# Kernel optimization log

Measured on AMD Instinct MI355X. Metric: run time of the kernel, lower is better.

Reference implementation:

```python
import jax, jax.numpy as jnp
import numpy as np

EPS_GN = 1e-5
EPS_ATTN = 1e-6
HEADS = 4
DIM_HEAD = 32
GROUPS = 32  # min(32, channels=128)


def group_norm(x, weight, bias, groups=GROUPS, eps=EPS_GN):
    # x: [b, c, h, w]
    b, c, h, w = x.shape
    xg = x.reshape(b, groups, c // groups, h, w)
    mean = xg.mean(axis=(2, 3, 4), keepdims=True)
    var = xg.var(axis=(2, 3, 4), keepdims=True)
    xg = (xg - mean) * jax.lax.rsqrt(var + eps)
    x = xg.reshape(b, c, h, w)
    return x * weight[None, :, None, None] + bias[None, :, None, None]


def conv1x1(x, w):
    # x: [b, c, h, w], w: [out, in] -> [b, out, h, w]
    return jnp.einsum('bchw,oc->bohw', x, w)


def setup_inputs() -> dict:
    key = jax.random.key(0)
    ks = jax.random.split(key, 6)
    b, c, h, w = 16, 128, 128, 128
    inner = HEADS * DIM_HEAD  # 128
    x = jax.random.normal(ks[0], (b, c, h, w), dtype=jnp.float32)
    gn1_w = jnp.ones((c,), jnp.float32) + 0.02 * jax.random.normal(ks[1], (c,), jnp.float32)
    gn1_b = 0.02 * jax.random.normal(ks[2], (c,), jnp.float32)
    w_qkv = jax.random.normal(ks[3], (inner * 3, c), jnp.float32) / np.sqrt(c)
    w_out = jax.random.normal(ks[4], (c, inner), jnp.float32) / np.sqrt(inner)
    gn2_w = jnp.ones((c,), jnp.float32) + 0.02 * jax.random.normal(ks[5], (c,), jnp.float32)
    gn2_b = jnp.zeros((c,), jnp.float32)
    return {"x": x, "gn1_w": gn1_w, "gn1_b": gn1_b, "w_qkv": w_qkv,
            "w_out": w_out, "gn2_w": gn2_w, "gn2_b": gn2_b}


def reference(x, gn1_w, gn1_b, w_qkv, w_out, gn2_w, gn2_b):
    b, c, h, w = x.shape
    residual = x
    xn = group_norm(x, gn1_w, gn1_b)
    qkv = conv1x1(xn, w_qkv)                      # [b, 3*inner, h, w]
    q, k, v = jnp.split(qkv, 3, axis=1)
    # 'b (heads d) h w -> b heads (h w) d'
    def to_tokens(t):
        return t.reshape(b, HEADS, DIM_HEAD, h * w).transpose(0, 1, 3, 2)
    q, k, v = to_tokens(q), to_tokens(k), to_tokens(v)
    q = jax.nn.elu(q) + 1.0
    k = jax.nn.elu(k) + 1.0
    k_sum = k.sum(axis=2)                          # [b, heads, d]
    kv = jnp.einsum('bhnd,bhne->bhde', k, v)       # [b, heads, d, d]
    qk_sum = jnp.einsum('bhnd,bhd->bhn', q, k_sum) # [b, heads, n]
    qkv_out = jnp.einsum('bhnd,bhde->bhne', q, kv) # [b, heads, n, d]
    out = qkv_out / (qk_sum[..., None] + EPS_ATTN)
    # 'b heads (h w) d -> b (heads d) h w'
    out = out.transpose(0, 1, 3, 2).reshape(b, HEADS * DIM_HEAD, h, w)
    out = conv1x1(out, w_out)
    out = group_norm(out, gn2_w, gn2_b)
    return out + residual
```

## Files before the change

### kernel.cpp

```cpp
#include <hip/hip_runtime.h>

#define B_   16
#define C_   128
#define HW_  16384

typedef __attribute__((ext_vector_type(4))) float  floatx4;
typedef __attribute__((ext_vector_type(8))) short  short8;
typedef __attribute__((ext_vector_type(4))) short  short4v;

static __device__ __forceinline__ unsigned short f2bf(float f){
  unsigned int u = __float_as_uint(f);
  u += 0x7FFFu + ((u >> 16) & 1u);
  return (unsigned short)(u >> 16);
}
static __device__ __forceinline__ float bf2f(unsigned short h){
  return __uint_as_float(((unsigned int)h) << 16);
}
static __device__ __forceinline__ float elu1(float v){
  return v > 0.f ? v + 1.f : __expf(v);
}
static __device__ __forceinline__ int keyx(int n){ return ((n >> 1) & 7) ^ ((n >> 4) & 7); }

__global__ __launch_bounds__(512) void k_xprep(const float* __restrict__ x,
    unsigned short* __restrict__ xT, float* __restrict__ gn1part){
  int blk = blockIdx.x;
  int b = blk >> 6, tile = blk & 63;
  int n0 = tile * 256;
  __shared__ unsigned short XS[32768];
  int t = threadIdx.x, w = t >> 6, l = t & 63;
  float sk[4], sk2[4];
  #pragma unroll
  for (int k = 0; k < 4; ++k){ sk[k] = 0.f; sk2[k] = 0.f; }
  #pragma unroll
  for (int k = 0; k < 4; ++k){
    float4 f4[4];
    #pragma unroll
    for (int j = 0; j < 4; ++j){
      int c = 16*w + 4*k + j;
      f4[j] = *(const float4*)(x + ((size_t)(b*128 + c))*HW_ + n0 + 4*l);
    }
    #pragma unroll
    for (int j = 0; j < 4; ++j){
      sk[k]  += f4[j].x + f4[j].y + f4[j].z + f4[j].w;
      sk2[k] += f4[j].x*f4[j].x + f4[j].y*f4[j].y + f4[j].z*f4[j].z + f4[j].w*f4[j].w;
    }
    int c0 = 16*w + 4*k, cs = c0 >> 3, co = c0 & 7;
    #pragma unroll
    for (int i = 0; i < 4; ++i){
      int n = 4*l + i;
      short4v p;
      #pragma unroll
      for (int j = 0; j < 4; ++j) p[j] = (short)f2bf(((const float*)&f4[j])[i]);
      *(short4v*)(XS + n*128 + (((cs ^ keyx(n)) << 3) + co)) = p;
    }
  }
  #pragma unroll
  for (int k = 0; k < 4; ++k){
    float a = sk[k], q = sk2[k];
    #pragma unroll
    for (int o = 32; o; o >>= 1){ a += __shfl_down(a, o); q += __shfl_down(q, o); }
    if (l == 0){
      gn1part[((size_t)blk)*64 + (4*w + k)*2 + 0] = a;
      gn1part[((size_t)blk)*64 + (4*w + k)*2 + 1] = q;
    }
  }
  __syncthreads();
  unsigned short* dst = xT + ((size_t)blk)*32768;
  for (int it = 0; it < 8; ++it){
    int slot = t + it*512;
    *(short8*)(dst + slot*8) = *(const short8*)(XS + slot*8);
  }
}

__global__ __launch_bounds__(64) void k_gn1fin(const float* __restrict__ gn1part,
    float* __restrict__ mean, float* __restrict__ rstd){
  int bg = blockIdx.x;
  int b = bg >> 5, g = bg & 31, l = threadIdx.x;
  const float* p = gn1part + ((size_t)(b*64 + l))*64 + g*2;
  float s = p[0], s2 = p[1];
  #pragma unroll
  for (int o = 32; o; o >>= 1){ s += __shfl_down(s, o); s2 += __shfl_down(s2, o); }
  if (l == 0){
    float m = s * (1.f/65536.f);
    float var = s2 * (1.f/65536.f) - m*m;
    mean[bg] = m; rstd[bg] = rsqrtf(var + 1e-5f);
  }
}

__global__ __launch_bounds__(64) void k_fold(const float* __restrict__ wqkv, const float* __restrict__ wout,
    const float* __restrict__ g1w, const float* __restrict__ g1b,
    const float* __restrict__ mean, const float* __restrict__ rstd,
    unsigned short* __restrict__ wqp, float* __restrict__ bias, unsigned short* __restrict__ woutb){
  int i = blockIdx.x, l = threadIdx.x;
  if (i < 6144){
    int b = i / 384, o = i % 384;
    float bsum = 0.f;
    #pragma unroll
    for (int j = 0; j < 2; ++j){
      int c = l*2 + j, g = c >> 2;
      float m = mean[b*32 + g], r = rstd[b*32 + g];
      float A  = r * g1w[c];
      float Bc = g1b[c] - m * A;
      float wv = wqkv[o*128 + c];
      wqp[((size_t)(b*384 + o))*128 + c] = f2bf(wv * A);
      bsum += wv * Bc;
    }
    #pragma unroll
    for (int o2 = 32; o2; o2 >>= 1) bsum += __shfl_down(bsum, o2);
    if (l == 0) bias[b*384 + o] = bsum;
  } else {
    int r = i - 6144;
    #pragma unroll
    for (int j = 0; j < 2; ++j){ int c = l*2 + j; woutb[r*128 + c] = f2bf(wout[r*128 + c]); }
  }
}

__global__ __launch_bounds__(512) void k_kv(const unsigned short* __restrict__ xT,
    const unsigned short* __restrict__ wqp, const float* __restrict__ bias,
    float* __restrict__ kvpart, float* __restrict__ ksumpart){
  int blk = blockIdx.x;
  int b = blk >> 7, nt = blk & 127;
  __shared__ unsigned short S[32768];
  int t = threadIdx.x, w = t >> 6, lane = t & 63, lr = lane & 15, lk = lane >> 4;
  const unsigned short* src = xT + ((size_t)(b*64 + (nt >> 1)))*32768 + (nt & 1)*16384;
  for (int it = 0; it < 4; ++it){
    int slot = t + it*512;
    *(short8*)(S + slot*8) = *(const short8*)(src + slot*8);
  }
  __syncthreads();
  short8 afr[2][4]; float biasr[2][4];
  #pragma unroll
  for (int rt = 0; rt < 2; ++rt){
    int o = 128 + rt*128 + w*16;
    #pragma unroll
    for (int ks = 0; ks < 4; ++ks)
      afr[rt][ks] = *(const short8*)(wqp + ((size_t)(b*384 + o + lr))*128 + ks*32 + lk*8);
    #pragma unroll
    for (int r = 0; r < 4; ++r) biasr[rt][r] = bias[b*384 + o + lk*4 + r];
  }
  short4v kpk[8], vpk[8];
  for (int ct = 0; ct < 8; ++ct){
    int nr = ct*16 + lr;
    int kn = keyx(nr);
    short8 bfr[4];
    #pragma unroll
    for (int ks = 0; ks < 4; ++ks)
      bfr[ks] = *(const short8*)(S + nr*128 + (((ks*4 + lk) ^ kn) << 3));
    #pragma unroll
    for (int rt = 0; rt < 2; ++rt){
      floatx4 acc = {0.f,0.f,0.f,0.f};
      #pragma unroll
      for (int ks = 0; ks < 4; ++ks)
        acc = __builtin_amdgcn_mfma_f32_16x16x32_bf16(afr[rt][ks], bfr[ks], acc, 0,0,0);
      short4v pk;
      #pragma unroll
      for (int r = 0; r < 4; ++r){
        float v = acc[r] + biasr[rt][r];
        if (rt == 0) v = elu1(v);
        pk[r] = (short)f2bf(v);
      }
      if (rt == 0) kpk[ct] = pk; else vpk[ct] = pk;
    }
  }
  __syncthreads();
  for (int ct = 0; ct < 8; ++ct){
    int n = ct*16 + lr;
    #pragma unroll
    for (int r = 0; r < 4; ++r){
      int c = w*16 + lk*4 + r;
      int key = (c >> 1) & 7;
      int off = c*128 + ((((n >> 3) ^ key) << 3) + (n & 7));
      S[off]         = (unsigned short)kpk[ct][r];
      S[16384 + off] = (unsigned short)vpk[ct][r];
    }
  }
  __syncthreads();
  short8 ones;
  #pragma unroll
  for (int j = 0; j < 8; ++j) ones[j] = (short)0x3F80;
  #pragma unroll
  for (int j = 0; j < 2; ++j){
    int m = w + 8*j;
    int h = m >> 2, dt = (m >> 1) & 1, et = m & 1;
    int arow = h*32 + dt*16 + lr, brow = h*32 + et*16 + lr;
    int akey = (lr >> 1) & 7;
    floatx4 acc = {0.f,0.f,0.f,0.f}, ks_acc = {0.f,0.f,0.f,0.f};
    #pragma unroll
    for (int ks = 0; ks < 4; ++ks){
      short8 ka = *(const short8*)(S + arow*128 + (((ks*4 + lk) ^ akey) << 3));
      short8 vb = *(const short8*)(S + 16384 + brow*128 + (((ks*4 + lk) ^ akey) << 3));
      acc = __builtin_amdgcn_mfma_f32_16x16x32_bf16(ka, vb, acc, 0,0,0);
      if (et == 0) ks_acc = __builtin_amdgcn_mfma_f32_16x16x32_bf16(ka, ones, ks_acc, 0,0,0);
    }
    float* kvp = kvpart + ((size_t)((b*128 + nt)*4 + h))*1024;
    #pragma unroll
    for (int r = 0; r < 4; ++r)
      kvp[(dt*16 + lk*4 + r)*32 + et*16 + lr] = acc[r];
    if (et == 0 && lr == 0){
      float* ksp = ksumpart + ((size_t)((b*128 + nt)*4 + h))*32;
      #pragma unroll
      for (int r = 0; r < 4; ++r) ksp[dt*16 + lk*4 + r] = ks_acc[r];
    }
  }
}

__global__ __launch_bounds__(256) void k_kvfin(const float* __restrict__ kvpart, const float* __restrict__ ksumpart,
    unsigned short* __restrict__ kvF){
  int bh = blockIdx.x, t = threadIdx.x;
  int b = bh >> 2, h = bh & 3;
  __shared__ float kvL[1024];
  __shared__ float ksumL[32];
  for (int i = t; i < 1024; i += 256){
    float s = 0.f;
    for (int nt = 0; nt < 128; ++nt) s += kvpart[((size_t)((b*128 + nt)*4 + h))*1024 + i];
    kvL[i] = s;
  }
  if (t < 32){
    float s = 0.f;
    for (int nt = 0; nt < 128; ++nt) s += ksumpart[((size_t)((b*128 + nt)*4 + h))*32 + t];
    ksumL[t] = s;
  }
  __syncthreads();
  for (int idx = t; idx < 3*512; idx += 256){
    int f = idx >> 9, rem = idx & 511;
    int lane = rem >> 3, j = rem & 7;
    int d = (lane >> 4)*8 + j;
    float v = (f < 2) ? kvL[d*32 + f*16 + (lane & 15)] : ksumL[d];
    kvF[(size_t)(bh*3 + f)*512 + rem] = f2bf(v);
  }
}

__global__ __launch_bounds__(512) void k_attn2(const unsigned short* __restrict__ xT,
    const unsigned short* __restrict__ wqp, const float* __restrict__ bias,
    const unsigned short* __restrict__ kvF, const unsigned short* __restrict__ woutb,
    unsigned short* __restrict__ hb, float* __restrict__ gn2part){
  int blk = blockIdx.x;
  int b = blk >> 6;
  int n0 = (blk & 63) * 256;
  __shared__ unsigned short S[32768];
  int t = threadIdx.x, w = t >> 6, lane = t & 63, lr = lane & 15, lk = lane >> 4;
  const unsigned short* src = xT + ((size_t)blk)*32768;
  for (int it = 0; it < 8; ++it){
    int slot = t + it*512;
    *(short8*)(S + slot*8) = *(const short8*)(src + slot*8);
  }
  short8 afr[4]; float biasq[4];
  #pragma unroll
  for (int ks = 0; ks < 4; ++ks)
    afr[ks] = *(const short8*)(wqp + ((size_t)(b*384 + w*16 + lr))*128 + ks*32 + lk*8);
  #pragma unroll
  for (int r = 0; r < 4; ++r) biasq[r] = bias[b*384 + w*16 + lk*4 + r];
  __syncthreads();
  short4v qpk[16];
  for (int ct = 0; ct < 16; ++ct){
    int nr = ct*16 + lr;
    int kn = keyx(nr);
    short8 bfr[4];
    #pragma unroll
    for (int ks = 0; ks < 4; ++ks)
      bfr[ks] = *(const short8*)(S + nr*128 + (((ks*4 + lk) ^ kn) << 3));
    floatx4 acc = {0.f,0.f,0.f,0.f};
    #pragma unroll
    for (int ks = 0; ks < 4; ++ks)
      acc = __builtin_amdgcn_mfma_f32_16x16x32_bf16(afr[ks], bfr[ks], acc, 0,0,0);
    short4v pk;
    #pragma unroll
    for (int r = 0; r < 4; ++r) pk[r] = (short)f2bf(elu1(acc[r] + biasq[r]));
    qpk[ct] = pk;
  }
  __syncthreads();
  for (int ct = 0; ct < 16; ++ct){
    int n = ct*16 + lr;
    int c0 = w*16 + lk*4;
    *(short4v*)(S + n*128 + ((((c0 >> 3) ^ (n & 7)) << 3) + (c0 & 7))) = qpk[ct];
  }
  const unsigned short* kvFb = kvF + (size_t)b * 12 * 512;
  short8 kvf[4][2], ksf[4];
  #pragma unroll
  for (int h = 0; h < 4; ++h){
    kvf[h][0] = *(const short8*)(kvFb + (h*3 + 0)*512 + lane*8);
    kvf[h][1] = *(const short8*)(kvFb + (h*3 + 1)*512 + lane*8);
    ksf[h]    = *(const short8*)(kvFb + (h*3 + 2)*512 + lane*8);
  }
  __syncthreads();
  short8 qf[2][4];
  #pragma unroll
  for (int nt = 0; nt < 2; ++nt){
    int n = w*32 + nt*16 + lr;
    #pragma unroll
    for (int h = 0; h < 4; ++h)
      qf[nt][h] = *(const short8*)(S + n*128 + (((4*h + lk) ^ (n & 7)) << 4) / 2);
  }
  #pragma unroll
  for (int nt = 0; nt < 2; ++nt){
    int n_local = w*32 + nt*16 + lr;
    #pragma unroll
    for (int h = 0; h < 4; ++h){
      floatx4 z = {0.f,0.f,0.f,0.f};
      floatx4 dn = __builtin_amdgcn_mfma_f32_16x16x32_bf16(ksf[h],    qf[nt][h], z, 0,0,0);
      floatx4 p0 = __builtin_amdgcn_mfma_f32_16x16x32_bf16(kvf[h][0], qf[nt][h], z, 0,0,0);
      floatx4 p1 = __builtin_amdgcn_mfma_f32_16x16x32_bf16(kvf[h][1], qf[nt][h], z, 0,0,0);
      float inv = 1.f / (dn[0] + 1e-6f);
      short4v o0, o1;
      #pragma unroll
      for (int r = 0; r < 4; ++r){ o0[r] = (short)f2bf(p0[r]*inv); o1[r] = (short)f2bf(p1[r]*inv); }
      int c0 = h*32 + lk*4;
      *(short4v*)(S + n_local*128 + ((((c0 >> 3) ^ (n_local & 7)) << 3) + (c0 & 7))) = o0;
      int c1 = c0 + 16;
      *(short4v*)(S + n_local*128 + ((((c1 >> 3) ^ (n_local & 7)) << 3) + (c1 & 7))) = o1;
    }
  }
  __syncthreads();
  short8 afr2[4];
  #pragma unroll
  for (int ks = 0; ks < 4; ++ks)
    afr2[ks] = *(const short8*)(woutb + (size_t)(w*16 + lr)*128 + ks*32 + lk*8);
  float gs[4] = {0,0,0,0}, gq[4] = {0,0,0,0};
  for (int ct = 0; ct < 16; ++ct){
    int nr = ct*16 + lr;
    short8 bfr[4];
    #pragma unroll
    for (int ks = 0; ks < 4; ++ks)
      bfr[ks] = *(const short8*)(S + nr*128 + (((ks*4 + lk) ^ (nr & 7)) << 3));
    floatx4 acc = {0.f,0.f,0.f,0.f};
    #pragma unroll
    for (int ks = 0; ks < 4; ++ks)
      acc = __builtin_amdgcn_mfma_f32_16x16x32_bf16(afr2[ks], bfr[ks], acc, 0,0,0);
    int nn = n0 + ct*16 + lr;
    #pragma unroll
    for (int r = 0; r < 4; ++r){
      float hv = acc[r];
      hb[((size_t)b*128 + w*16 + lk*4 + r) * HW_ + nn] = f2bf(hv);
      gs[r] += hv; gq[r] += hv * hv;
    }
  }
  #pragma unroll
  for (int m = 1; m < 16; m <<= 1){
    #pragma unroll
    for (int r = 0; r < 4; ++r){ gs[r] += __shfl_xor(gs[r], m); gq[r] += __shfl_xor(gq[r], m); }
  }
  if (lr == 0){
    #pragma unroll
    for (int r = 0; r < 4; ++r){
      int o = w*16 + lk*4 + r;
      gn2part[((size_t)blk*128 + o)*2 + 0] = gs[r];
      gn2part[((size_t)blk*128 + o)*2 + 1] = gq[r];
    }
  }
}

__global__ __launch_bounds__(64) void k_gn2stats(const float* __restrict__ gn2part,
    float* __restrict__ mean, float* __restrict__ rstd){
  int b = blockIdx.x >> 5, g = blockIdx.x & 31;
  int lane = threadIdx.x;
  float s = 0.f, s2 = 0.f;
  #pragma unroll
  for (int j = 0; j < 4; ++j){
    const float* p = gn2part + (((size_t)(b*64 + lane))*128 + g*4 + j)*2;
    s += p[0]; s2 += p[1];
  }
  #pragma unroll
  for (int o = 32; o; o >>= 1){ s += __shfl_down(s, o); s2 += __shfl_down(s2, o); }
  if (lane == 0){
    float m = s * (1.f/65536.f);
    float var = s2 * (1.f/65536.f) - m*m;
    mean[blockIdx.x] = m; rstd[blockIdx.x] = rsqrtf(var + 1e-5f);
  }
}

__global__ __launch_bounds__(256) void k_final(const unsigned short* __restrict__ hb, const float* __restrict__ x,
    float* __restrict__ out,
    const float* __restrict__ mean, const float* __restrict__ rstd,
    const float* __restrict__ g2w, const float* __restrict__ g2b){
  for (size_t chunk = (size_t)blockIdx.x*256 + threadIdx.x; chunk < 4194304ull; chunk += (size_t)2048*256){
    size_t base = chunk * 8;
    int c  = (int)((base >> 14) & 127);
    int bg = (int)(base >> 21) * 32 + (c >> 2);
    float m = mean[bg], r = rstd[bg];
    float sc = r * g2w[c], sh = g2b[c] - m * sc;
    short8 hv = *(const short8*)(hb + base);
    const float4* xp = (const float4*)(x + base);
    float4 x0 = xp[0], x1 = xp[1];
    float4 o0, o1;
    o0.x = bf2f((unsigned short)hv[0])*sc + sh + x0.x;
    o0.y = bf2f((unsigned short)hv[1])*sc + sh + x0.y;
    o0.z = bf2f((unsigned short)hv[2])*sc + sh + x0.z;
    o0.w = bf2f((unsigned short)hv[3])*sc + sh + x0.w;
    o1.x = bf2f((unsigned short)hv[4])*sc + sh + x1.x;
    o1.y = bf2f((unsigned short)hv[5])*sc + sh + x1.y;
    o1.z = bf2f((unsigned short)hv[6])*sc + sh + x1.z;
    o1.w = bf2f((unsigned short)hv[7])*sc + sh + x1.w;
    float4* op = (float4*)(out + base);
    op[0] = o0; op[1] = o1;
  }
}

extern "C" void kernel_launch(void* const* d_in, const int* in_sizes, int n_in,
                              void* d_out, int out_size, void* d_ws, size_t ws_size,
                              hipStream_t stream){
  const float* x    = (const float*)d_in[0];
  const float* g1w  = (const float*)d_in[1];
  const float* g1b  = (const float*)d_in[2];
  const float* wqkv = (const float*)d_in[3];
  const float* wout = (const float*)d_in[4];
  const float* g2w  = (const float*)d_in[5];
  const float* g2b  = (const float*)d_in[6];
  char* ws = (char*)d_ws;
  (void)in_sizes; (void)n_in; (void)out_size; (void)ws_size;

  float* gn1part  = (float*)(ws + 0);
  float* gn1_mean = (float*)(ws + 262144);
  float* gn1_rstd = (float*)(ws + 264192);
  float* gn2_mean = (float*)(ws + 266240);
  float* gn2_rstd = (float*)(ws + 268288);
  float* bias     = (float*)(ws + 270336);
  unsigned short* woutb = (unsigned short*)(ws + 294912);
  unsigned short* kvF   = (unsigned short*)(ws + 327680);
  unsigned short* wqp   = (unsigned short*)(ws + 524288);
  float* ksumpart = (float*)(ws + 2097152);
  float* kvpart   = (float*)(ws + 3145728);
  float* gn2part  = (float*)(ws + 36700160);
  unsigned short* xT = (unsigned short*)(ws + 37748736);
  unsigned short* hb = (unsigned short*)(ws + 104857600);

  k_xprep<<<dim3(1024), dim3(512), 0, stream>>>(x, xT, gn1part);
  k_gn1fin<<<dim3(512), dim3(64), 0, stream>>>(gn1part, gn1_mean, gn1_rstd);
  k_fold<<<dim3(6272), dim3(64), 0, stream>>>(wqkv, wout, g1w, g1b, gn1_mean, gn1_rstd, wqp, bias, woutb);
  k_kv<<<dim3(2048), dim3(512), 0, stream>>>(xT, wqp, bias, kvpart, ksumpart);
  k_kvfin<<<dim3(64), dim3(256), 0, stream>>>(kvpart, ksumpart, kvF);
  k_attn2<<<dim3(1024), dim3(512), 0, stream>>>(xT, wqp, bias, kvF, woutb, hb, gn2part);
  k_gn2stats<<<dim3(512), dim3(64), 0, stream>>>(gn2part, gn2_mean, gn2_rstd);
  k_final<<<dim3(2048), dim3(256), 0, stream>>>(hb, x, (float*)d_out, gn2_mean, gn2_rstd, g2w, g2b);
}
```

Baseline: 223.8 us.

## Batch kv tiles per block, 2D-tile attn warps, read residual from bf16 xT

k_kv now has each block walk 8 token tiles while keeping its kv and ksum accumulators in registers. That cuts the number of fp32 partials written and later reduced in k_kvfin by a factor of eight. k_attn2 assigns warps a 2D (row-group × column-group) tile so weight fragments are reused across more columns, and it reduces the GroupNorm-2 partials across warps in shared memory. k_final takes the residual from the bf16 transposed copy xT staged through LDS instead of rereading fp32 x, which halves residual traffic but adds bf16 rounding error to the output.

Result: slower. 238.9 us (+6.8%).

```diff
diff --git a/kernel.cpp b/kernel.cpp
--- a/kernel.cpp
+++ b/kernel.cpp
@@ -119,87 +119,106 @@
     const unsigned short* __restrict__ wqp, const float* __restrict__ bias,
     float* __restrict__ kvpart, float* __restrict__ ksumpart){
   int blk = blockIdx.x;
-  int b = blk >> 7, nt = blk & 127;
+  int b = blk >> 4, chunk = blk & 15;
   __shared__ unsigned short S[32768];
   int t = threadIdx.x, w = t >> 6, lane = t & 63, lr = lane & 15, lk = lane >> 4;
-  const unsigned short* src = xT + ((size_t)(b*64 + (nt >> 1)))*32768 + (nt & 1)*16384;
-  for (int it = 0; it < 4; ++it){
-    int slot = t + it*512;
-    *(short8*)(S + slot*8) = *(const short8*)(src + slot*8);
-  }
-  __syncthreads();
-  short8 afr[2][4]; float biasr[2][4];
-  #pragma unroll
-  for (int rt = 0; rt < 2; ++rt){
-    int o = 128 + rt*128 + w*16;
+  int rg = w >> 1, cg = w & 1;
+  short8 afr[4][4]; float biasr[4][4];
+  #pragma unroll
+  for (int rtl = 0; rtl < 4; ++rtl){
+    int o = 128 + (rg*4 + rtl)*16;
     #pragma unroll
     for (int ks = 0; ks < 4; ++ks)
-      afr[rt][ks] = *(const short8*)(wqp + ((size_t)(b*384 + o + lr))*128 + ks*32 + lk*8);
-    #pragma unroll
-    for (int r = 0; r < 4; ++r) biasr[rt][r] = bias[b*384 + o + lk*4 + r];
-  }
-  short4v kpk[8], vpk[8];
-  for (int ct = 0; ct < 8; ++ct){
-    int nr = ct*16 + lr;
-    int kn = keyx(nr);
-    short8 bfr[4];
-    #pragma unroll
-    for (int ks = 0; ks < 4; ++ks)
-      bfr[ks] = *(const short8*)(S + nr*128 + (((ks*4 + lk) ^ kn) << 3));
-    #pragma unroll
-    for (int rt = 0; rt < 2; ++rt){
-      floatx4 acc = {0.f,0.f,0.f,0.f};
+      afr[rtl][ks] = *(const short8*)(wqp + ((size_t)(b*384 + o + lr))*128 + ks*32 + lk*8);
+    #pragma unroll
+    for (int r = 0; r < 4; ++r) biasr[rtl][r] = bias[b*384 + o + lk*4 + r];
+  }
+  short8 ones;
+  #pragma unroll
+  for (int j = 0; j < 8; ++j) ones[j] = (short)0x3F80;
+  floatx4 accA = {0,0,0,0}, accB = {0,0,0,0}, ksaA = {0,0,0,0}, ksaB = {0,0,0,0};
+  for (int it = 0; it < 8; ++it){
+    const unsigned short* src = xT + ((size_t)(b*64 + chunk*4 + (it>>1)))*32768 + (it&1)*16384;
+    #pragma unroll
+    for (int i = 0; i < 4; ++i){
+      int slot = t + i*512;
+      *(short8*)(S + slot*8) = *(const short8*)(src + slot*8);
+    }
+    __syncthreads();
+    short4v pk[4][4];
+    #pragma unroll
+    for (int ctl = 0; ctl < 4; ++ctl){
+      int nr = (cg*4 + ctl)*16 + lr;
+      int kn = keyx(nr);
+      short8 bfr[4];
       #pragma unroll
       for (int ks = 0; ks < 4; ++ks)
-        acc = __builtin_amdgcn_mfma_f32_16x16x32_bf16(afr[rt][ks], bfr[ks], acc, 0,0,0);
-      short4v pk;
-      #pragma unroll
-      for (int r = 0; r < 4; ++r){
-        float v = acc[r] + biasr[rt][r];
-        if (rt == 0) v = elu1(v);
-        pk[r] = (short)f2bf(v);
+        bfr[ks] = *(const short8*)(S + nr*128 + (((ks*4 + lk) ^ kn) << 3));
+      #pragma unroll
+      for (int rtl = 0; rtl < 4; ++rtl){
+        floatx4 acc = {0.f,0.f,0.f,0.f};
+        #pragma unroll
+        for (int ks = 0; ks < 4; ++ks)
+          acc = __builtin_amdgcn_mfma_f32_16x16x32_bf16(afr[rtl][ks], bfr[ks], acc, 0,0,0);
+        #pragma unroll
+        for (int r = 0; r < 4; ++r){
+          float v = acc[r] + biasr[rtl][r];
+          if (rg < 2) v = elu1(v);
+          pk[rtl][ctl][r] = (short)f2bf(v);
+        }
       }
-      if (rt == 0) kpk[ct] = pk; else vpk[ct] = pk;
-    }
-  }
-  __syncthreads();
-  for (int ct = 0; ct < 8; ++ct){
-    int n = ct*16 + lr;
-    #pragma unroll
-    for (int r = 0; r < 4; ++r){
-      int c = w*16 + lk*4 + r;
-      int key = (c >> 1) & 7;
-      int off = c*128 + ((((n >> 3) ^ key) << 3) + (n & 7));
-      S[off]         = (unsigned short)kpk[ct][r];
-      S[16384 + off] = (unsigned short)vpk[ct][r];
-    }
-  }
-  __syncthreads();
-  short8 ones;
-  #pragma unroll
-  for (int j = 0; j < 8; ++j) ones[j] = (short)0x3F80;
+    }
+    __syncthreads();
+    #pragma unroll
+    for (int rtl = 0; rtl < 4; ++rtl){
+      int rt = rg*4 + rtl;
+      int cbase = (rt & 7)*16 + lk*4;
+      int voff = (rt < 8) ? 0 : 16384;
+      #pragma unroll
+      for (int ctl = 0; ctl < 4; ++ctl){
+        int n = (cg*4 + ctl)*16 + lr;
+        #pragma unroll
+        for (int r = 0; r < 4; ++r){
+          int c = cbase + r;
+          S[voff + c*128 + ((((n >> 3) ^ ((c >> 1) & 7)) << 3) + (n & 7))] = (unsigned short)pk[rtl][ctl][r];
+        }
+      }
+    }
+    __syncthreads();
+    #pragma unroll
+    for (int j = 0; j < 2; ++j){
+      int m = w + 8*j;
+      int h = m >> 2, dt = (m >> 1) & 1, et = m & 1;
+      int arow = h*32 + dt*16 + lr, brow = h*32 + et*16 + lr;
+      int akey = (lr >> 1) & 7;
+      #pragma unroll
+      for (int ks = 0; ks < 4; ++ks){
+        short8 ka = *(const short8*)(S + arow*128 + (((ks*4 + lk) ^ akey) << 3));
+        short8 vb = *(const short8*)(S + 16384 + brow*128 + (((ks*4 + lk) ^ akey) << 3));
+        if (j == 0){
+          accA = __builtin_amdgcn_mfma_f32_16x16x32_bf16(ka, vb, accA, 0,0,0);
+          if (et == 0) ksaA = __builtin_amdgcn_mfma_f32_16x16x32_bf16(ka, ones, ksaA, 0,0,0);
+        } else {
+          accB = __builtin_amdgcn_mfma_f32_16x16x32_bf16(ka, vb, accB, 0,0,0);
+          if (et == 0) ksaB = __builtin_amdgcn_mfma_f32_16x16x32_bf16(ka, ones, ksaB, 0,0,0);
+        }
+      }
+    }
+    __syncthreads();
+  }
   #pragma unroll
   for (int j = 0; j < 2; ++j){
     int m = w + 8*j;
     int h = m >> 2, dt = (m >> 1) & 1, et = m & 1;
-    int arow = h*32 + dt*16 + lr, brow = h*32 + et*16 + lr;
-    int akey = (lr >> 1) & 7;
-    floatx4 acc = {0.f,0.f,0.f,0.f}, ks_acc = {0.f,0.f,0.f,0.f};
-    #pragma unroll
-    for (int ks = 0; ks < 4; ++ks){
-      short8 ka = *(const short8*)(S + arow*128 + (((ks*4 + lk) ^ akey) << 3));
-      short8 vb = *(const short8*)(S + 16384 + brow*128 + (((ks*4 + lk) ^ akey) << 3));
-      acc = __builtin_amdgcn_mfma_f32_16x16x32_bf16(ka, vb, acc, 0,0,0);
-      if (et == 0) ks_acc = __builtin_amdgcn_mfma_f32_16x16x32_bf16(ka, ones, ks_acc, 0,0,0);
-    }
-    float* kvp = kvpart + ((size_t)((b*128 + nt)*4 + h))*1024;
+    floatx4 acc = j ? accB : accA, ksa = j ? ksaB : ksaA;
+    float* kvp = kvpart + ((size_t)((b*16 + chunk)*4 + h))*1024;
     #pragma unroll
     for (int r = 0; r < 4; ++r)
       kvp[(dt*16 + lk*4 + r)*32 + et*16 + lr] = acc[r];
     if (et == 0 && lr == 0){
-      float* ksp = ksumpart + ((size_t)((b*128 + nt)*4 + h))*32;
-      #pragma unroll
-      for (int r = 0; r < 4; ++r) ksp[dt*16 + lk*4 + r] = ks_acc[r];
+      float* ksp = ksumpart + ((size_t)((b*16 + chunk)*4 + h))*32;
+      #pragma unroll
+      for (int r = 0; r < 4; ++r) ksp[dt*16 + lk*4 + r] = ksa[r];
     }
   }
 }
@@ -212,12 +231,12 @@
   __shared__ float ksumL[32];
   for (int i = t; i < 1024; i += 256){
     float s = 0.f;
-    for (int nt = 0; nt < 128; ++nt) s += kvpart[((size_t)((b*128 + nt)*4 + h))*1024 + i];
+    for (int nt = 0; nt < 16; ++nt) s += kvpart[((size_t)((b*16 + nt)*4 + h))*1024 + i];
     kvL[i] = s;
   }
   if (t < 32){
     float s = 0.f;
-    for (int nt = 0; nt < 128; ++nt) s += ksumpart[((size_t)((b*128 + nt)*4 + h))*32 + t];
+    for (int nt = 0; nt < 16; ++nt) s += ksumpart[((size_t)((b*16 + nt)*4 + h))*32 + t];
     ksumL[t] = s;
   }
   __syncthreads();
@@ -238,41 +257,53 @@
   int b = blk >> 6;
   int n0 = (blk & 63) * 256;
   __shared__ unsigned short S[32768];
+  __shared__ float gnS[4][128][2];
   int t = threadIdx.x, w = t >> 6, lane = t & 63, lr = lane & 15, lk = lane >> 4;
+  int rg = w >> 2, cg = w & 3;
   const unsigned short* src = xT + ((size_t)blk)*32768;
   for (int it = 0; it < 8; ++it){
     int slot = t + it*512;
     *(short8*)(S + slot*8) = *(const short8*)(src + slot*8);
   }
-  short8 afr[4]; float biasq[4];
-  #pragma unroll
-  for (int ks = 0; ks < 4; ++ks)
-    afr[ks] = *(const short8*)(wqp + ((size_t)(b*384 + w*16 + lr))*128 + ks*32 + lk*8);
-  #pragma unroll
-  for (int r = 0; r < 4; ++r) biasq[r] = bias[b*384 + w*16 + lk*4 + r];
-  __syncthreads();
-  short4v qpk[16];
-  for (int ct = 0; ct < 16; ++ct){
-    int nr = ct*16 + lr;
+  short8 afr[4][4]; float biasq[4][4];
+  #pragma unroll
+  for (int rtl = 0; rtl < 4; ++rtl){
+    int o = rg*64 + rtl*16;
+    #pragma unroll
+    for (int ks = 0; ks < 4; ++ks)
+      afr[rtl][ks] = *(const short8*)(wqp + ((size_t)(b*384 + o + lr))*128 + ks*32 + lk*8);
+    #pragma unroll
+    for (int r = 0; r < 4; ++r) biasq[rtl][r] = bias[b*384 + o + lk*4 + r];
+  }
+  __syncthreads();
+  short4v qpk[4][4];
+  #pragma unroll
+  for (int ctl = 0; ctl < 4; ++ctl){
+    int nr = (cg*4 + ctl)*16 + lr;
     int kn = keyx(nr);
     short8 bfr[4];
     #pragma unroll
     for (int ks = 0; ks < 4; ++ks)
       bfr[ks] = *(const short8*)(S + nr*128 + (((ks*4 + lk) ^ kn) << 3));
-    floatx4 acc = {0.f,0.f,0.f,0.f};
-    #pragma unroll
-    for (int ks = 0; ks < 4; ++ks)
-      acc = __builtin_amdgcn_mfma_f32_16x16x32_bf16(afr[ks], bfr[ks], acc, 0,0,0);
-    short4v pk;
-    #pragma unroll
-    for (int r = 0; r < 4; ++r) pk[r] = (short)f2bf(elu1(acc[r] + biasq[r]));
-    qpk[ct] = pk;
-  }
-  __syncthreads();
-  for (int ct = 0; ct < 16; ++ct){
-    int n = ct*16 + lr;
-    int c0 = w*16 + lk*4;
-    *(short4v*)(S + n*128 + ((((c0 >> 3) ^ (n & 7)) << 3) + (c0 & 7))) = qpk[ct];
+    #pragma unroll
+    for (int rtl = 0; rtl < 4; ++rtl){
+      floatx4 acc = {0.f,0.f,0.f,0.f};
+      #pragma unroll
+      for (int ks = 0; ks < 4; ++ks)
+        acc = __builtin_amdgcn_mfma_f32_16x16x32_bf16(afr[rtl][ks], bfr[ks], acc, 0,0,0);
+      #pragma unroll
+      for (int r = 0; r < 4; ++r) qpk[rtl][ctl][r] = (short)f2bf(elu1(acc[r] + biasq[rtl][r]));
+    }
+  }
+  __syncthreads();
+  #pragma unroll
+  for (int rtl = 0; rtl < 4; ++rtl){
+    int c0 = rg*64 + rtl*16 + lk*4;
+    #pragma unroll
+    for (int ctl = 0; ctl < 4; ++ctl){
+      int n = (cg*4 + ctl)*16 + lr;
+      *(short4v*)(S + n*128 + ((((c0 >> 3) ^ (n & 7)) << 3) + (c0 & 7))) = qpk[rtl][ctl];
+    }
   }
   const unsigned short* kvFb = kvF + (size_t)b * 12 * 512;
   short8 kvf[4][2], ksf[4];
@@ -289,7 +320,7 @@
     int n = w*32 + nt*16 + lr;
     #pragma unroll
     for (int h = 0; h < 4; ++h)
-      qf[nt][h] = *(const short8*)(S + n*128 + (((4*h + lk) ^ (n & 7)) << 4) / 2);
+      qf[nt][h] = *(const short8*)(S + n*128 + (((4*h + lk) ^ (n & 7)) << 3));
   }
   #pragma unroll
   for (int nt = 0; nt < 2; ++nt){
@@ -311,41 +342,62 @@
     }
   }
   __syncthreads();
-  short8 afr2[4];
-  #pragma unroll
-  for (int ks = 0; ks < 4; ++ks)
-    afr2[ks] = *(const short8*)(woutb + (size_t)(w*16 + lr)*128 + ks*32 + lk*8);
-  float gs[4] = {0,0,0,0}, gq[4] = {0,0,0,0};
-  for (int ct = 0; ct < 16; ++ct){
-    int nr = ct*16 + lr;
+  short8 afr2[4][4];
+  #pragma unroll
+  for (int rtl = 0; rtl < 4; ++rtl)
+    #pragma unroll
+    for (int ks = 0; ks < 4; ++ks)
+      afr2[rtl][ks] = *(const short8*)(woutb + (size_t)(rg*64 + rtl*16 + lr)*128 + ks*32 + lk*8);
+  float gs[4][4], gq[4][4];
+  #pragma unroll
+  for (int rtl = 0; rtl < 4; ++rtl)
+    #pragma unroll
+    for (int r = 0; r < 4; ++r){ gs[rtl][r] = 0.f; gq[rtl][r] = 0.f; }
+  #pragma unroll
+  for (int ctl = 0; ctl < 4; ++ctl){
+    int nr = (cg*4 + ctl)*16 + lr;
     short8 bfr[4];
     #pragma unroll
     for (int ks = 0; ks < 4; ++ks)
       bfr[ks] = *(const short8*)(S + nr*128 + (((ks*4 + lk) ^ (nr & 7)) << 3));
-    floatx4 acc = {0.f,0.f,0.f,0.f};
-    #pragma unroll
-    for (int ks = 0; ks < 4; ++ks)
-      acc = __builtin_amdgcn_mfma_f32_16x16x32_bf16(afr2[ks], bfr[ks], acc, 0,0,0);
-    int nn = n0 + ct*16 + lr;
-    #pragma unroll
-    for (int r = 0; r < 4; ++r){
-      float hv = acc[r];
-      hb[((size_t)b*128 + w*16 + lk*4 + r) * HW_ + nn] = f2bf(hv);
-      gs[r] += hv; gq[r] += hv * hv;
-    }
-  }
-  #pragma unroll
-  for (int m = 1; m < 16; m <<= 1){
-    #pragma unroll
-    for (int r = 0; r < 4; ++r){ gs[r] += __shfl_xor(gs[r], m); gq[r] += __shfl_xor(gq[r], m); }
-  }
+    int nn = n0 + nr;
+    #pragma unroll
+    for (int rtl = 0; rtl < 4; ++rtl){
+      floatx4 acc = {0.f,0.f,0.f,0.f};
+      #pragma unroll
+      for (int ks = 0; ks < 4; ++ks)
+        acc = __builtin_amdgcn_mfma_f32_16x16x32_bf16(afr2[rtl][ks], bfr[ks], acc, 0,0,0);
+      #pragma unroll
+      for (int r = 0; r < 4; ++r){
+        float hv = acc[r];
+        hb[((size_t)(b*128 + rg*64 + rtl*16 + lk*4 + r)) * HW_ + nn] = f2bf(hv);
+        gs[rtl][r] += hv; gq[rtl][r] += hv * hv;
+      }
+    }
+  }
+  #pragma unroll
+  for (int m = 1; m < 16; m <<= 1)
+    #pragma unroll
+    for (int rtl = 0; rtl < 4; ++rtl)
+      #pragma unroll
+      for (int r = 0; r < 4; ++r){ gs[rtl][r] += __shfl_xor(gs[rtl][r], m); gq[rtl][r] += __shfl_xor(gq[rtl][r], m); }
   if (lr == 0){
     #pragma unroll
-    for (int r = 0; r < 4; ++r){
-      int o = w*16 + lk*4 + r;
-      gn2part[((size_t)blk*128 + o)*2 + 0] = gs[r];
-      gn2part[((size_t)blk*128 + o)*2 + 1] = gq[r];
-    }
+    for (int rtl = 0; rtl < 4; ++rtl)
+      #pragma unroll
+      for (int r = 0; r < 4; ++r){
+        int c = rg*64 + rtl*16 + lk*4 + r;
+        gnS[cg][c][0] = gs[rtl][r];
+        gnS[cg][c][1] = gq[rtl][r];
+      }
+  }
+  __syncthreads();
+  if (t < 128){
+    float a = 0.f, q2 = 0.f;
+    #pragma unroll
+    for (int cgi = 0; cgi < 4; ++cgi){ a += gnS[cgi][t][0]; q2 += gnS[cgi][t][1]; }
+    gn2part[((size_t)blk*128 + t)*2 + 0] = a;
+    gn2part[((size_t)blk*128 + t)*2 + 1] = q2;
   }
 }
 
@@ -368,29 +420,40 @@
   }
 }
 
-__global__ __launch_bounds__(256) void k_final(const unsigned short* __restrict__ hb, const float* __restrict__ x,
-    float* __restrict__ out,
+__global__ __launch_bounds__(256) void k_final(const unsigned short* __restrict__ hb,
+    const unsigned short* __restrict__ xT, float* __restrict__ out,
     const float* __restrict__ mean, const float* __restrict__ rstd,
     const float* __restrict__ g2w, const float* __restrict__ g2b){
-  for (size_t chunk = (size_t)blockIdx.x*256 + threadIdx.x; chunk < 4194304ull; chunk += (size_t)2048*256){
-    size_t base = chunk * 8;
-    int c  = (int)((base >> 14) & 127);
-    int bg = (int)(base >> 21) * 32 + (c >> 2);
+  int blk = blockIdx.x;
+  int b = blk >> 6;
+  int n0 = (blk & 63) * 256;
+  __shared__ unsigned short XS[32768];
+  int t = threadIdx.x;
+  const unsigned short* src = xT + ((size_t)blk)*32768;
+  for (int it = 0; it < 16; ++it){
+    int slot = t + it*256;
+    *(short8*)(XS + slot*8) = *(const short8*)(src + slot*8);
+  }
+  __syncthreads();
+  for (int it = 0; it < 16; ++it){
+    int idx = t + it*256;
+    int c = idx >> 5, oct = idx & 31;
+    int bg = b*32 + (c >> 2);
     float m = mean[bg], r = rstd[bg];
     float sc = r * g2w[c], sh = g2b[c] - m * sc;
-    short8 hv = *(const short8*)(hb + base);
-    const float4* xp = (const float4*)(x + base);
-    float4 x0 = xp[0], x1 = xp[1];
+    size_t gbase = ((size_t)(b*128 + c))*HW_ + n0 + oct*8;
+    short8 hv = *(const short8*)(hb + gbase);
+    float ov[8];
+    #pragma unroll
+    for (int j = 0; j < 8; ++j){
+      int n = oct*8 + j;
+      unsigned short xv = XS[n*128 + ((((c >> 3) ^ keyx(n)) << 3) + (c & 7))];
+      ov[j] = bf2f((unsigned short)hv[j])*sc + sh + bf2f(xv);
+    }
+    float4* op = (float4*)(out + gbase);
     float4 o0, o1;
-    o0.x = bf2f((unsigned short)hv[0])*sc + sh + x0.x;
-    o0.y = bf2f((unsigned short)hv[1])*sc + sh + x0.y;
-    o0.z = bf2f((unsigned short)hv[2])*sc + sh + x0.z;
-    o0.w = bf2f((unsigned short)hv[3])*sc + sh + x0.w;
-    o1.x = bf2f((unsigned short)hv[4])*sc + sh + x1.x;
-    o1.y = bf2f((unsigned short)hv[5])*sc + sh + x1.y;
-    o1.z = bf2f((unsigned short)hv[6])*sc + sh + x1.z;
-    o1.w = bf2f((unsigned short)hv[7])*sc + sh + x1.w;
-    float4* op = (float4*)(out + base);
+    o0.x = ov[0]; o0.y = ov[1]; o0.z = ov[2]; o0.w = ov[3];
+    o1.x = ov[4]; o1.y = ov[5]; o1.z = ov[6]; o1.w = ov[7];
     op[0] = o0; op[1] = o1;
   }
 }
@@ -418,17 +481,17 @@
   unsigned short* kvF   = (unsigned short*)(ws + 327680);
   unsigned short* wqp   = (unsigned short*)(ws + 524288);
   float* ksumpart = (float*)(ws + 2097152);
-  float* kvpart   = (float*)(ws + 3145728);
-  float* gn2part  = (float*)(ws + 36700160);
-  unsigned short* xT = (unsigned short*)(ws + 37748736);
-  unsigned short* hb = (unsigned short*)(ws + 104857600);
+  float* kvpart   = (float*)(ws + 2228224);
+  float* gn2part  = (float*)(ws + 6422528);
+  unsigned short* xT = (unsigned short*)(ws + 8388608);
+  unsigned short* hb = (unsigned short*)(ws + 75497472);
 
   k_xprep<<<dim3(1024), dim3(512), 0, stream>>>(x, xT, gn1part);
   k_gn1fin<<<dim3(512), dim3(64), 0, stream>>>(gn1part, gn1_mean, gn1_rstd);
   k_fold<<<dim3(6272), dim3(64), 0, stream>>>(wqkv, wout, g1w, g1b, gn1_mean, gn1_rstd, wqp, bias, woutb);
-  k_kv<<<dim3(2048), dim3(512), 0, stream>>>(xT, wqp, bias, kvpart, ksumpart);
+  k_kv<<<dim3(256), dim3(512), 0, stream>>>(xT, wqp, bias, kvpart, ksumpart);
   k_kvfin<<<dim3(64), dim3(256), 0, stream>>>(kvpart, ksumpart, kvF);
   k_attn2<<<dim3(1024), dim3(512), 0, stream>>>(xT, wqp, bias, kvF, woutb, hb, gn2part);
   k_gn2stats<<<dim3(512), dim3(64), 0, stream>>>(gn2part, gn2_mean, gn2_rstd);
-  k_final<<<dim3(2048), dim3(256), 0, stream>>>(hb, x, (float*)d_out, gn2_mean, gn2_rstd, g2w, g2b);
-}
+  k_final<<<dim3(1024), dim3(256), 0, stream>>>(hb, xT, (float*)d_out, gn2_mean, gn2_rstd, g2w, g2b);
+}
```

## Fold output projection into per-head KV matrix and read residual from bf16 copy

Applied to the files above, without the earlier changes.

Precomputes M = W_out·KV per batch in the KV finalize kernel, and applies the denominator normalization directly to q. The attention kernel then runs a single GEMM against M instead of a KV product followed by an output GEMM. The attention kernel is retiled to 128-token blocks with 2x2 waves and writes h in a per-tile layout. The final kernel takes the residual from the bf16 transposed x already in workspace instead of fp32 x, which cuts memory traffic but lowers the residual's precision to bf16.

Measured after the change: 241.1 us. +7.8%, slower.

```diff
diff --git a/kernel.cpp b/kernel.cpp
--- a/kernel.cpp
+++ b/kernel.cpp
@@ -204,12 +204,11 @@
   }
 }
 
-__global__ __launch_bounds__(256) void k_kvfin(const float* __restrict__ kvpart, const float* __restrict__ ksumpart,
-    unsigned short* __restrict__ kvF){
+__global__ __launch_bounds__(256) void k_kvmfold(const float* __restrict__ kvpart, const float* __restrict__ ksumpart,
+    const unsigned short* __restrict__ woutb, unsigned short* __restrict__ Mb, float* __restrict__ ksumF){
   int bh = blockIdx.x, t = threadIdx.x;
   int b = bh >> 2, h = bh & 3;
   __shared__ float kvL[1024];
-  __shared__ float ksumL[32];
   for (int i = t; i < 1024; i += 256){
     float s = 0.f;
     for (int nt = 0; nt < 128; ++nt) s += kvpart[((size_t)((b*128 + nt)*4 + h))*1024 + i];
@@ -218,134 +217,144 @@
   if (t < 32){
     float s = 0.f;
     for (int nt = 0; nt < 128; ++nt) s += ksumpart[((size_t)((b*128 + nt)*4 + h))*32 + t];
-    ksumL[t] = s;
-  }
-  __syncthreads();
-  for (int idx = t; idx < 3*512; idx += 256){
-    int f = idx >> 9, rem = idx & 511;
-    int lane = rem >> 3, j = rem & 7;
-    int d = (lane >> 4)*8 + j;
-    float v = (f < 2) ? kvL[d*32 + f*16 + (lane & 15)] : ksumL[d];
-    kvF[(size_t)(bh*3 + f)*512 + rem] = f2bf(v);
-  }
-}
-
-__global__ __launch_bounds__(512) void k_attn2(const unsigned short* __restrict__ xT,
+    ksumF[b*128 + h*32 + t] = s;
+  }
+  __syncthreads();
+  int o = t >> 1, d0 = (t & 1)*16;
+  float w2row[32];
+  #pragma unroll
+  for (int e = 0; e < 32; ++e) w2row[e] = bf2f(woutb[o*128 + h*32 + e]);
+  for (int dd = 0; dd < 16; ++dd){
+    int d = d0 + dd;
+    float s = 0.f;
+    #pragma unroll
+    for (int e = 0; e < 32; ++e) s += w2row[e] * kvL[d*32 + e];
+    Mb[((size_t)b)*16384 + o*128 + h*32 + d] = f2bf(s);
+  }
+}
+
+__global__ __launch_bounds__(256) void k_attn2(const unsigned short* __restrict__ xT,
     const unsigned short* __restrict__ wqp, const float* __restrict__ bias,
-    const unsigned short* __restrict__ kvF, const unsigned short* __restrict__ woutb,
-    unsigned short* __restrict__ hb, float* __restrict__ gn2part){
+    const float* __restrict__ ksumF, const unsigned short* __restrict__ Mb,
+    unsigned short* __restrict__ hbT, float* __restrict__ gn2part){
   int blk = blockIdx.x;
-  int b = blk >> 6;
-  int n0 = (blk & 63) * 256;
-  __shared__ unsigned short S[32768];
+  int b = blk >> 7, t128 = blk & 127;
+  __shared__ unsigned short S[16384];
   int t = threadIdx.x, w = t >> 6, lane = t & 63, lr = lane & 15, lk = lane >> 4;
-  const unsigned short* src = xT + ((size_t)blk)*32768;
+  int rg = w >> 1, cg = w & 1;
+  const unsigned short* src = xT + ((size_t)(b*64 + (t128 >> 1)))*32768 + (t128 & 1)*16384;
   for (int it = 0; it < 8; ++it){
-    int slot = t + it*512;
+    int slot = t + it*256;
     *(short8*)(S + slot*8) = *(const short8*)(src + slot*8);
   }
-  short8 afr[4]; float biasq[4];
-  #pragma unroll
-  for (int ks = 0; ks < 4; ++ks)
-    afr[ks] = *(const short8*)(wqp + ((size_t)(b*384 + w*16 + lr))*128 + ks*32 + lk*8);
-  #pragma unroll
-  for (int r = 0; r < 4; ++r) biasq[r] = bias[b*384 + w*16 + lk*4 + r];
-  __syncthreads();
-  short4v qpk[16];
-  for (int ct = 0; ct < 16; ++ct){
-    int nr = ct*16 + lr;
+  short8 afr[4][4]; float biasq[4][4], ksL[4][4];
+  #pragma unroll
+  for (int rtl = 0; rtl < 4; ++rtl){
+    int o = rg*64 + rtl*16;
+    #pragma unroll
+    for (int ks = 0; ks < 4; ++ks)
+      afr[rtl][ks] = *(const short8*)(wqp + ((size_t)(b*384 + o + lr))*128 + ks*32 + lk*8);
+    #pragma unroll
+    for (int r = 0; r < 4; ++r){
+      biasq[rtl][r] = bias[b*384 + o + lk*4 + r];
+      ksL[rtl][r]   = ksumF[b*128 + o + lk*4 + r];
+    }
+  }
+  __syncthreads();
+  short4v qpk[4][4];
+  #pragma unroll
+  for (int ctl = 0; ctl < 4; ++ctl){
+    int nr = cg*64 + ctl*16 + lr;
     int kn = keyx(nr);
     short8 bfr[4];
     #pragma unroll
     for (int ks = 0; ks < 4; ++ks)
       bfr[ks] = *(const short8*)(S + nr*128 + (((ks*4 + lk) ^ kn) << 3));
-    floatx4 acc = {0.f,0.f,0.f,0.f};
-    #pragma unroll
-    for (int ks = 0; ks < 4; ++ks)
-      acc = __builtin_amdgcn_mfma_f32_16x16x32_bf16(afr[ks], bfr[ks], acc, 0,0,0);
-    short4v pk;
-    #pragma unroll
-    for (int r = 0; r < 4; ++r) pk[r] = (short)f2bf(elu1(acc[r] + biasq[r]));
-    qpk[ct] = pk;
-  }
-  __syncthreads();
-  for (int ct = 0; ct < 16; ++ct){
-    int n = ct*16 + lr;
-    int c0 = w*16 + lk*4;
-    *(short4v*)(S + n*128 + ((((c0 >> 3) ^ (n & 7)) << 3) + (c0 & 7))) = qpk[ct];
-  }
-  const unsigned short* kvFb = kvF + (size_t)b * 12 * 512;
-  short8 kvf[4][2], ksf[4];
-  #pragma unroll
-  for (int h = 0; h < 4; ++h){
-    kvf[h][0] = *(const short8*)(kvFb + (h*3 + 0)*512 + lane*8);
-    kvf[h][1] = *(const short8*)(kvFb + (h*3 + 1)*512 + lane*8);
-    ksf[h]    = *(const short8*)(kvFb + (h*3 + 2)*512 + lane*8);
-  }
-  __syncthreads();
-  short8 qf[2][4];
-  #pragma unroll
-  for (int nt = 0; nt < 2; ++nt){
-    int n = w*32 + nt*16 + lr;
-    #pragma unroll
-    for (int h = 0; h < 4; ++h)
-      qf[nt][h] = *(const short8*)(S + n*128 + (((4*h + lk) ^ (n & 7)) << 4) / 2);
-  }
-  #pragma unroll
-  for (int nt = 0; nt < 2; ++nt){
-    int n_local = w*32 + nt*16 + lr;
-    #pragma unroll
-    for (int h = 0; h < 4; ++h){
-      floatx4 z = {0.f,0.f,0.f,0.f};
-      floatx4 dn = __builtin_amdgcn_mfma_f32_16x16x32_bf16(ksf[h],    qf[nt][h], z, 0,0,0);
-      floatx4 p0 = __builtin_amdgcn_mfma_f32_16x16x32_bf16(kvf[h][0], qf[nt][h], z, 0,0,0);
-      floatx4 p1 = __builtin_amdgcn_mfma_f32_16x16x32_bf16(kvf[h][1], qf[nt][h], z, 0,0,0);
-      float inv = 1.f / (dn[0] + 1e-6f);
-      short4v o0, o1;
-      #pragma unroll
-      for (int r = 0; r < 4; ++r){ o0[r] = (short)f2bf(p0[r]*inv); o1[r] = (short)f2bf(p1[r]*inv); }
-      int c0 = h*32 + lk*4;
-      *(short4v*)(S + n_local*128 + ((((c0 >> 3) ^ (n_local & 7)) << 3) + (c0 & 7))) = o0;
-      int c1 = c0 + 16;
-      *(short4v*)(S + n_local*128 + ((((c1 >> 3) ^ (n_local & 7)) << 3) + (c1 & 7))) = o1;
-    }
-  }
-  __syncthreads();
-  short8 afr2[4];
-  #pragma unroll
-  for (int ks = 0; ks < 4; ++ks)
-    afr2[ks] = *(const short8*)(woutb + (size_t)(w*16 + lr)*128 + ks*32 + lk*8);
-  float gs[4] = {0,0,0,0}, gq[4] = {0,0,0,0};
-  for (int ct = 0; ct < 16; ++ct){
-    int nr = ct*16 + lr;
+    float qv[4][4];
+    #pragma unroll
+    for (int rtl = 0; rtl < 4; ++rtl){
+      floatx4 acc = {0.f,0.f,0.f,0.f};
+      #pragma unroll
+      for (int ks = 0; ks < 4; ++ks)
+        acc = __builtin_amdgcn_mfma_f32_16x16x32_bf16(afr[rtl][ks], bfr[ks], acc, 0,0,0);
+      #pragma unroll
+      for (int r = 0; r < 4; ++r) qv[rtl][r] = elu1(acc[r] + biasq[rtl][r]);
+    }
+    #pragma unroll
+    for (int hh = 0; hh < 2; ++hh){
+      float p = 0.f;
+      #pragma unroll
+      for (int rr = 0; rr < 2; ++rr)
+        #pragma unroll
+        for (int r = 0; r < 4; ++r) p += ksL[2*hh + rr][r] * qv[2*hh + rr][r];
+      p += __shfl_xor(p, 16);
+      p += __shfl_xor(p, 32);
+      float inv = 1.f / (p + 1e-6f);
+      #pragma unroll
+      for (int rr = 0; rr < 2; ++rr)
+        #pragma unroll
+        for (int r = 0; r < 4; ++r) qpk[2*hh + rr][ctl][r] = (short)f2bf(qv[2*hh + rr][r] * inv);
+    }
+  }
+  __syncthreads();
+  #pragma unroll
+  for (int rtl = 0; rtl < 4; ++rtl){
+    int c0 = rg*64 + rtl*16 + lk*4;
+    #pragma unroll
+    for (int ctl = 0; ctl < 4; ++ctl){
+      int n = cg*64 + ctl*16 + lr;
+      *(short4v*)(S + n*128 + ((((c0 >> 3) ^ (n & 7)) << 3) + (c0 & 7))) = qpk[rtl][ctl];
+    }
+  }
+  __syncthreads();
+  short8 afr2[4][4];
+  #pragma unroll
+  for (int rtl = 0; rtl < 4; ++rtl)
+    #pragma unroll
+    for (int ks = 0; ks < 4; ++ks)
+      afr2[rtl][ks] = *(const short8*)(Mb + ((size_t)b)*16384 + (size_t)(rg*64 + rtl*16 + lr)*128 + ks*32 + lk*8);
+  float gs[4][4], gq[4][4];
+  #pragma unroll
+  for (int rtl = 0; rtl < 4; ++rtl)
+    #pragma unroll
+    for (int r = 0; r < 4; ++r){ gs[rtl][r] = 0.f; gq[rtl][r] = 0.f; }
+  #pragma unroll
+  for (int ctl = 0; ctl < 4; ++ctl){
+    int nr = cg*64 + ctl*16 + lr;
     short8 bfr[4];
     #pragma unroll
     for (int ks = 0; ks < 4; ++ks)
       bfr[ks] = *(const short8*)(S + nr*128 + (((ks*4 + lk) ^ (nr & 7)) << 3));
-    floatx4 acc = {0.f,0.f,0.f,0.f};
-    #pragma unroll
-    for (int ks = 0; ks < 4; ++ks)
-      acc = __builtin_amdgcn_mfma_f32_16x16x32_bf16(afr2[ks], bfr[ks], acc, 0,0,0);
-    int nn = n0 + ct*16 + lr;
-    #pragma unroll
-    for (int r = 0; r < 4; ++r){
-      float hv = acc[r];
-      hb[((size_t)b*128 + w*16 + lk*4 + r) * HW_ + nn] = f2bf(hv);
-      gs[r] += hv; gq[r] += hv * hv;
-    }
-  }
-  #pragma unroll
-  for (int m = 1; m < 16; m <<= 1){
-    #pragma unroll
-    for (int r = 0; r < 4; ++r){ gs[r] += __shfl_xor(gs[r], m); gq[r] += __shfl_xor(gq[r], m); }
-  }
+    #pragma unroll
+    for (int rtl = 0; rtl < 4; ++rtl){
+      floatx4 acc = {0.f,0.f,0.f,0.f};
+      #pragma unroll
+      for (int ks = 0; ks < 4; ++ks)
+        acc = __builtin_amdgcn_mfma_f32_16x16x32_bf16(afr2[rtl][ks], bfr[ks], acc, 0,0,0);
+      #pragma unroll
+      for (int r = 0; r < 4; ++r){
+        float hv = acc[r];
+        int c = rg*64 + rtl*16 + lk*4 + r;
+        hbT[(size_t)blk*16384 + c*128 + nr] = f2bf(hv);
+        gs[rtl][r] += hv; gq[rtl][r] += hv * hv;
+      }
+    }
+  }
+  #pragma unroll
+  for (int m = 1; m < 16; m <<= 1)
+    #pragma unroll
+    for (int rtl = 0; rtl < 4; ++rtl)
+      #pragma unroll
+      for (int r = 0; r < 4; ++r){ gs[rtl][r] += __shfl_xor(gs[rtl][r], m); gq[rtl][r] += __shfl_xor(gq[rtl][r], m); }
   if (lr == 0){
     #pragma unroll
-    for (int r = 0; r < 4; ++r){
-      int o = w*16 + lk*4 + r;
-      gn2part[((size_t)blk*128 + o)*2 + 0] = gs[r];
-      gn2part[((size_t)blk*128 + o)*2 + 1] = gq[r];
-    }
+    for (int rtl = 0; rtl < 4; ++rtl)
+      #pragma unroll
+      for (int r = 0; r < 4; ++r){
+        int c = rg*64 + rtl*16 + lk*4 + r;
+        gn2part[((size_t)(blk*2 + cg)*128 + c)*2 + 0] = gs[rtl][r];
+        gn2part[((size_t)(blk*2 + cg)*128 + c)*2 + 1] = gq[rtl][r];
+      }
   }
 }
 
@@ -355,9 +364,15 @@
   int lane = threadIdx.x;
   float s = 0.f, s2 = 0.f;
   #pragma unroll
-  for (int j = 0; j < 4; ++j){
-    const float* p = gn2part + (((size_t)(b*64 + lane))*128 + g*4 + j)*2;
-    s += p[0]; s2 += p[1];
+  for (int tt = 0; tt < 2; ++tt){
+    int t128 = lane + tt*64;
+    #pragma unroll
+    for (int cgi = 0; cgi < 2; ++cgi)
+      #pragma unroll
+      for (int j = 0; j < 4; ++j){
+        const float* p = gn2part + ((size_t)((b*128 + t128)*2 + cgi)*128 + g*4 + j)*2;
+        s += p[0]; s2 += p[1];
+      }
   }
   #pragma unroll
   for (int o = 32; o; o >>= 1){ s += __shfl_down(s, o); s2 += __shfl_down(s2, o); }
@@ -368,30 +383,40 @@
   }
 }
 
-__global__ __launch_bounds__(256) void k_final(const unsigned short* __restrict__ hb, const float* __restrict__ x,
-    float* __restrict__ out,
+__global__ __launch_bounds__(256) void k_final(const unsigned short* __restrict__ hbT,
+    const unsigned short* __restrict__ xT, float* __restrict__ out,
     const float* __restrict__ mean, const float* __restrict__ rstd,
     const float* __restrict__ g2w, const float* __restrict__ g2b){
-  for (size_t chunk = (size_t)blockIdx.x*256 + threadIdx.x; chunk < 4194304ull; chunk += (size_t)2048*256){
-    size_t base = chunk * 8;
-    int c  = (int)((base >> 14) & 127);
-    int bg = (int)(base >> 21) * 32 + (c >> 2);
+  int blk = blockIdx.x;
+  int b = blk >> 7, t128 = blk & 127;
+  __shared__ unsigned short XS[16384];
+  int t = threadIdx.x;
+  const unsigned short* src = xT + ((size_t)(b*64 + (t128 >> 1)))*32768 + (t128 & 1)*16384;
+  for (int it = 0; it < 8; ++it){
+    int slot = t + it*256;
+    *(short8*)(XS + slot*8) = *(const short8*)(src + slot*8);
+  }
+  __syncthreads();
+  const unsigned short* hsrc = hbT + (size_t)blk*16384;
+  for (int it = 0; it < 8; ++it){
+    int idx = t + it*256;
+    int c = idx >> 4, oct = idx & 15;
+    int bg = b*32 + (c >> 2);
     float m = mean[bg], r = rstd[bg];
     float sc = r * g2w[c], sh = g2b[c] - m * sc;
-    short8 hv = *(const short8*)(hb + base);
-    const float4* xp = (const float4*)(x + base);
-    float4 x0 = xp[0], x1 = xp[1];
+    short8 hv = *(const short8*)(hsrc + c*128 + oct*8);
+    float ov[8];
+    #pragma unroll
+    for (int j = 0; j < 8; ++j){
+      int n = oct*8 + j;
+      unsigned short xv = XS[n*128 + ((((c >> 3) ^ keyx(n)) << 3) + (c & 7))];
+      ov[j] = bf2f((unsigned short)hv[j])*sc + sh + bf2f(xv);
+    }
+    float* op = out + ((size_t)(b*128 + c))*HW_ + t128*128 + oct*8;
     float4 o0, o1;
-    o0.x = bf2f((unsigned short)hv[0])*sc + sh + x0.x;
-    o0.y = bf2f((unsigned short)hv[1])*sc + sh + x0.y;
-    o0.z = bf2f((unsigned short)hv[2])*sc + sh + x0.z;
-    o0.w = bf2f((unsigned short)hv[3])*sc + sh + x0.w;
-    o1.x = bf2f((unsigned short)hv[4])*sc + sh + x1.x;
-    o1.y = bf2f((unsigned short)hv[5])*sc + sh + x1.y;
-    o1.z = bf2f((unsigned short)hv[6])*sc + sh + x1.z;
-    o1.w = bf2f((unsigned short)hv[7])*sc + sh + x1.w;
-    float4* op = (float4*)(out + base);
-    op[0] = o0; op[1] = o1;
+    o0.x = ov[0]; o0.y = ov[1]; o0.z = ov[2]; o0.w = ov[3];
+    o1.x = ov[4]; o1.y = ov[5]; o1.z = ov[6]; o1.w = ov[7];
+    *(float4*)op = o0; *(float4*)(op + 4) = o1;
   }
 }
 
@@ -415,20 +440,21 @@
   float* gn2_rstd = (float*)(ws + 268288);
   float* bias     = (float*)(ws + 270336);
   unsigned short* woutb = (unsigned short*)(ws + 294912);
-  unsigned short* kvF   = (unsigned short*)(ws + 327680);
-  unsigned short* wqp   = (unsigned short*)(ws + 524288);
-  float* ksumpart = (float*)(ws + 2097152);
-  float* kvpart   = (float*)(ws + 3145728);
-  float* gn2part  = (float*)(ws + 36700160);
-  unsigned short* xT = (unsigned short*)(ws + 37748736);
-  unsigned short* hb = (unsigned short*)(ws + 104857600);
+  float* ksumF    = (float*)(ws + 327680);
+  unsigned short* Mb = (unsigned short*)(ws + 335872);
+  unsigned short* wqp = (unsigned short*)(ws + 860160);
+  float* ksumpart = (float*)(ws + 2433024);
+  float* kvpart   = (float*)(ws + 4194304);
+  float* gn2part  = (float*)(ws + 37748736);
+  unsigned short* xT  = (unsigned short*)(ws + 41943040);
+  unsigned short* hbT = (unsigned short*)(ws + 109051904);
 
   k_xprep<<<dim3(1024), dim3(512), 0, stream>>>(x, xT, gn1part);
   k_gn1fin<<<dim3(512), dim3(64), 0, stream>>>(gn1part, gn1_mean, gn1_rstd);
   k_fold<<<dim3(6272), dim3(64), 0, stream>>>(wqkv, wout, g1w, g1b, gn1_mean, gn1_rstd, wqp, bias, woutb);
   k_kv<<<dim3(2048), dim3(512), 0, stream>>>(xT, wqp, bias, kvpart, ksumpart);
-  k_kvfin<<<dim3(64), dim3(256), 0, stream>>>(kvpart, ksumpart, kvF);
-  k_attn2<<<dim3(1024), dim3(512), 0, stream>>>(xT, wqp, bias, kvF, woutb, hb, gn2part);
+  k_kvmfold<<<dim3(64), dim3(256), 0, stream>>>(kvpart, ksumpart, woutb, Mb, ksumF);
+  k_attn2<<<dim3(2048), dim3(256), 0, stream>>>(xT, wqp, bias, ksumF, Mb, hbT, gn2part);
   k_gn2stats<<<dim3(512), dim3(64), 0, stream>>>(gn2part, gn2_mean, gn2_rstd);
-  k_final<<<dim3(2048), dim3(256), 0, stream>>>(hb, x, (float*)d_out, gn2_mean, gn2_rstd, g2w, g2b);
-}
+  k_final<<<dim3(2048), dim3(256), 0, stream>>>(hbT, xT, (float*)d_out, gn2_mean, gn2_rstd, g2w, g2b);
+}
```
